# Kernel tuning notes

Hardware: AMD Instinct MI355X
Metric: run time of the kernel (lower is better)

The kernel has to match this reference:

```python
import jax, jax.numpy as jnp
import numpy as np

I = 256  # input size
H = 256  # hidden size
B = 128
S = 1024
EPS = 1e-5


def setup_inputs() -> dict:
    key = jax.random.key(0)
    ks = jax.random.split(key, 8)
    bound = 1.0 / np.sqrt(H)
    x = jax.random.normal(ks[0], (B, S, I), dtype=jnp.float32)
    mask = jax.random.randint(ks[1], (B, S), 0, 2) == 1
    W_ih = jax.random.uniform(ks[2], (4 * H, I), jnp.float32, -bound, bound)
    W_hh = jax.random.uniform(ks[3], (4 * H, H), jnp.float32, -bound, bound)
    b_ih = jax.random.uniform(ks[4], (4 * H,), jnp.float32, -bound, bound)
    b_hh = jax.random.uniform(ks[5], (4 * H,), jnp.float32, -bound, bound)
    gamma = jnp.ones((H,), jnp.float32)
    beta = jnp.zeros((H,), jnp.float32)
    return {"x": x, "mask": mask, "W_ih": W_ih, "W_hh": W_hh,
            "b_ih": b_ih, "b_hh": b_hh, "gamma": gamma, "beta": beta}


def _layernorm(h, gamma, beta):
    mu = jnp.mean(h, axis=-1, keepdims=True)
    var = jnp.var(h, axis=-1, keepdims=True)
    return (h - mu) * jax.lax.rsqrt(var + EPS) * gamma + beta


def reference(x, mask, W_ih, W_hh, b_ih, b_hh, gamma, beta):
    b = x.shape[0]
    h0 = jnp.zeros((b, H), x.dtype)
    c0 = jnp.zeros((b, H), x.dtype)
    out0 = jnp.zeros((b, H), x.dtype)

    def step(carry, inp):
        h, c, out = carry
        x_t, m_t = inp  # (B,I), (B,)
        hn = _layernorm(h, gamma, beta)
        gates = x_t @ W_ih.T + b_ih + hn @ W_hh.T + b_hh  # (B,4H)
        i_g, f_g, g_g, o_g = jnp.split(gates, 4, axis=-1)
        c = jax.nn.sigmoid(f_g) * c + jax.nn.sigmoid(i_g) * jnp.tanh(g_g)
        h = jax.nn.sigmoid(o_g) * jnp.tanh(c)
        # output[~mask] = h[~mask]; where mask is True the old output is kept
        out = jnp.where(m_t[:, None], out, h)
        return (h, c, out), None

    xs = (jnp.swapaxes(x, 0, 1), jnp.swapaxes(mask, 0, 1))  # (S,B,I), (S,B)
    (h, c, out), _ = jax.lax.scan(step, (h0, c0, out0), xs)
    return out
```

## Files before the change

### kernel.cpp

```cpp
#include <hip/hip_runtime.h>
#include <hip/hip_bf16.h>
#include <stdint.h>


#define Bb 128
#define Ss 1024
#define Ii 256
#define Hh 256
#define G4v 1024
#define EPSF 1e-5f

typedef __bf16 bf16;
typedef _Float16 f16;
typedef __attribute__((ext_vector_type(8))) __bf16 bf16x8;
typedef __attribute__((ext_vector_type(4))) __bf16 bf16x4;
typedef __attribute__((ext_vector_type(8))) _Float16 f16x8;
typedef __attribute__((ext_vector_type(4))) _Float16 f16x4;
typedef __attribute__((ext_vector_type(4))) float f32x4;
typedef unsigned int u32;
typedef unsigned long long u64;

static __device__ __forceinline__ f32x4 mfma16b(bf16x8 a, bf16x8 b, f32x4 c) {
  return __builtin_amdgcn_mfma_f32_16x16x32_bf16(a, b, c, 0, 0, 0);
}
static __device__ __forceinline__ f32x4 mfma16h(f16x8 a, f16x8 b, f32x4 c) {
  return __builtin_amdgcn_mfma_f32_16x16x32_f16(a, b, c, 0, 0, 0);
}
static __device__ __forceinline__ float sigm(float x) { return 1.0f / (1.0f + __expf(-x)); }
static __device__ __forceinline__ float tanhf_(float x) {
  float e = __expf(-2.0f * fabsf(x));
  float t = (1.0f - e) / (1.0f + e);
  return x < 0.0f ? -t : t;
}
static __device__ __forceinline__ unsigned short ush(f16 h) {
  return __builtin_bit_cast(unsigned short, h);
}
static __device__ __forceinline__ f16 hus(unsigned short u) {
  return __builtin_bit_cast(f16, u);
}

__global__ void k_conv_wih(const float* __restrict__ W, bf16* __restrict__ hi,
                           bf16* __restrict__ lo) {
  int i = (blockIdx.x * 256 + threadIdx.x) * 4;
  f32x4 v = *(const f32x4*)(W + i);
  bf16x4 h_, l_;
#pragma unroll
  for (int j = 0; j < 4; ++j) {
    bf16 hh = (bf16)v[j];
    h_[j] = hh;
    l_[j] = (bf16)(v[j] - (float)hh);
  }
  *(bf16x4*)(hi + i) = h_;
  *(bf16x4*)(lo + i) = l_;
}

__global__ void k_prep_whh(const float* __restrict__ W, const float* __restrict__ gamma,
                           f16* __restrict__ Wf) {
  int tid = blockIdx.x * 256 + threadIdx.x;
  int lane = tid & 63;
  int fk = tid >> 6;
  int ntg = fk >> 3, kt = fk & 7;
  int g = ntg * 16 + (lane & 15);
  int k = kt * 32 + ((lane >> 4) << 3);
  f16x8 r;
#pragma unroll
  for (int j = 0; j < 8; ++j) r[j] = (f16)(W[g * Hh + k + j] * gamma[k + j]);
  *(f16x8*)(Wf + (size_t)tid * 8) = r;
}

__global__ void k_prep_rd(const float* __restrict__ W, const float* __restrict__ gamma,
                          const float* __restrict__ beta, const float* __restrict__ bih,
                          const float* __restrict__ bhh, float* __restrict__ RD) {
  int g = blockIdx.x * 256 + threadIdx.x;
  float r = 0.f, d = 0.f;
  for (int k = 0; k < Hh; ++k) {
    float w = W[g * Hh + k];
    r += w * gamma[k];
    d += w * beta[k];
  }
  RD[2 * g] = r;
  RD[2 * g + 1] = d + bih[g] + bhh[g];
}

__global__ __launch_bounds__(256, 2) void k_gemm(const float* __restrict__ x,
                                                 const bf16* __restrict__ Whi,
                                                 const bf16* __restrict__ Wlo,
                                                 float* __restrict__ xw,
                                                 int t0, int Tc, int ntb) {
  __shared__ bf16 Bs[2][128 * 128];
  int bid = blockIdx.x;
  int b = bid & 127;
  int r2 = bid >> 7;
  int tb = r2 % ntb;
  int gt = r2 / ntb;
  int g0 = gt * 128;
  int tid = threadIdx.x, w = tid >> 6, lane = tid & 63;
  int li = lane & 15, lg = lane >> 4;
  char* BsB = (char*)Bs;
  int tbase = tb * 128 + 32 * w;
  f32x4 acc[2][8];
#pragma unroll
  for (int mt = 0; mt < 2; ++mt)
#pragma unroll
    for (int nt = 0; nt < 8; ++nt) acc[mt][nt] = (f32x4){0.f, 0.f, 0.f, 0.f};

  for (int kp = 0; kp < 2; ++kp) {
#pragma unroll
    for (int it = 0; it < 8; ++it) {
      int p = it * 4096 + tid * 16;
      int row = p >> 8, colb = p & 255;
      size_t goff = (size_t)(g0 + row) * 512 + kp * 256 + colb;
      int dst = row * 256 + (colb ^ ((row & 7) << 4));
      *(bf16x8*)(BsB + dst) = *(const bf16x8*)((const char*)Whi + goff);
      *(bf16x8*)(BsB + 32768 + dst) = *(const bf16x8*)((const char*)Wlo + goff);
    }
    __syncthreads();
#pragma unroll
    for (int kt = 0; kt < 4; ++kt) {
      int kl = kt * 32 + lg * 8;
      int kgl = kp * 128 + kl;
      bf16x8 ah[2], al[2];
#pragma unroll
      for (int mt = 0; mt < 2; ++mt) {
        int t = t0 + tbase + 16 * mt + li;
        const float* xp = x + ((size_t)b * Ss + t) * Ii + kgl;
        f32x4 f0 = *(const f32x4*)xp;
        f32x4 f1 = *(const f32x4*)(xp + 4);
        bf16x8 hv, lv;
#pragma unroll
        for (int j = 0; j < 4; ++j) {
          bf16 h0 = (bf16)f0[j];
          hv[j] = h0;
          lv[j] = (bf16)(f0[j] - (float)h0);
          bf16 h1 = (bf16)f1[j];
          hv[4 + j] = h1;
          lv[4 + j] = (bf16)(f1[j] - (float)h1);
        }
        ah[mt] = hv;
        al[mt] = lv;
      }
#pragma unroll
      for (int nt = 0; nt < 8; ++nt) {
        int grow = nt * 16 + li;
        int off = grow * 256 + ((kl * 2) ^ ((grow & 7) << 4));
        bf16x8 bh = *(const bf16x8*)(BsB + off);
        bf16x8 bl = *(const bf16x8*)(BsB + 32768 + off);
#pragma unroll
        for (int mt = 0; mt < 2; ++mt) {
          acc[mt][nt] = mfma16b(ah[mt], bh, acc[mt][nt]);
          acc[mt][nt] = mfma16b(ah[mt], bl, acc[mt][nt]);
          acc[mt][nt] = mfma16b(al[mt], bh, acc[mt][nt]);
        }
      }
    }
    __syncthreads();
  }
#pragma unroll
  for (int mt = 0; mt < 2; ++mt)
#pragma unroll
    for (int nt = 0; nt < 8; ++nt)
#pragma unroll
      for (int r = 0; r < 4; ++r) {
        int tl = tbase + 16 * mt + lg * 4 + r;
        int g = g0 + nt * 16 + li;
        xw[((size_t)b * Tc + tl) * G4v + g] = acc[mt][nt][r];
      }
}

__global__ __launch_bounds__(256, 1) void k_recur(
    const f16* __restrict__ Wf, const float* __restrict__ xw,
    const int* __restrict__ mask, const float* __restrict__ RD,
    float* __restrict__ st_h, float* __restrict__ st_c, float* __restrict__ st_o,
    u64* pub, float* __restrict__ out, int t0, int Tc, int first, int last) {
  __shared__ f16 hb[2][16 * 256];
  __shared__ float murs[2][16][2];
  __shared__ float2 spw[4][16];
  __shared__ float spart[16][16][2];
  int bid = blockIdx.x;
  int grp = bid & 7, q = bid >> 3;
  int tid = threadIdx.x, w = tid >> 6, lane = tid & 63;
  int li = lane & 15, lg = lane >> 4;
  int b0 = grp * 16;
  int jloc = (q * 4 + w) * 16 + li;
  char* hbB = (char*)hb;

  f16x8 wp[4][8];
#pragma unroll
  for (int c = 0; c < 4; ++c)
#pragma unroll
    for (int kt = 0; kt < 8; ++kt) {
      int ntg = c * 16 + q * 4 + w;
      wp[c][kt] = *(const f16x8*)(Wf + ((size_t)(ntg * 8 + kt) * 64 + lane) * 8);
      asm volatile("" : "+a"(wp[c][kt]));
    }
  float Rr[4], Dd[4];
#pragma unroll
  for (int c = 0; c < 4; ++c) {
    int g = c * 256 + jloc;
    Rr[c] = RD[2 * g];
    Dd[c] = RD[2 * g + 1];
  }

  float cst[4], ost[4];
  if (first) {
#pragma unroll
    for (int i = 0; i < 16; ++i) {
      hb[0][tid * 16 + i] = (f16)0.0f;
      hb[1][tid * 16 + i] = (f16)0.0f;
    }
#pragma unroll
    for (int r = 0; r < 4; ++r) { cst[r] = 0.f; ost[r] = 0.f; }
    if (tid < 16) { murs[0][tid][0] = 0.f; murs[0][tid][1] = rsqrtf(EPSF); }
  } else {
    int row = tid >> 4, cs = tid & 15, jseg = cs * 16;
    float s = 0.f, ss = 0.f;
#pragma unroll
    for (int i = 0; i < 16; ++i) {
      float v = st_h[(size_t)(b0 + row) * Hh + jseg + i];
      s += v;
      ss += v * v;
      f16 hh = (f16)v;
      int boff = row * 512 + (((jseg + i) * 2) ^ ((row & 7) << 4));
      *(f16*)(hbB + boff) = hh;
      *(f16*)(hbB + 8192 + boff) = (f16)(v - (float)hh);
    }
    spart[row][cs][0] = s;
    spart[row][cs][1] = ss;
#pragma unroll
    for (int r = 0; r < 4; ++r) {
      int m = lg * 4 + r;
      cst[r] = st_c[(size_t)(b0 + m) * Hh + jloc];
      ost[r] = st_o[(size_t)(b0 + m) * Hh + jloc];
    }
    __syncthreads();
    if (tid < 16) {
      float s2 = 0.f, ss2 = 0.f;
#pragma unroll
      for (int i = 0; i < 16; ++i) { s2 += spart[tid][i][0]; ss2 += spart[tid][i][1]; }
      float mu = s2 * (1.f / 256.f);
      float var = ss2 * (1.f / 256.f) - mu * mu;
      float rs = rsqrtf(var + EPSF);
      murs[0][tid][0] = mu * rs;
      murs[0][tid][1] = rs;
    }
  }
  __syncthreads();

  float xwv[4][4];
  int mk[4];
#pragma unroll
  for (int c = 0; c < 4; ++c)
#pragma unroll
    for (int r = 0; r < 4; ++r)
      xwv[c][r] = xw[((size_t)(b0 + lg * 4 + r) * Tc + 0) * G4v + c * 256 + jloc];
#pragma unroll
  for (int r = 0; r < 4; ++r) mk[r] = mask[(size_t)(b0 + lg * 4 + r) * Ss + t0];

  int grow = tid >> 4, gcg = tid & 15;

  for (int tl = 0; tl < Tc; ++tl) {
    int tg = t0 + tl;
    int slot = (tg + 1) & 1;
    u32 want = (u32)(tg + 1);

    f32x4 a0[4], a1[4];
#pragma unroll
    for (int c = 0; c < 4; ++c) {
      a0[c] = (f32x4){0.f, 0.f, 0.f, 0.f};
      a1[c] = (f32x4){0.f, 0.f, 0.f, 0.f};
    }
#pragma unroll
    for (int kt = 0; kt < 8; ++kt) {
      int aoff = li * 512 + (((kt * 32 + lg * 8) * 2) ^ ((li & 7) << 4));
      f16x8 ah = *(const f16x8*)(hbB + aoff);
      f16x8 al = *(const f16x8*)(hbB + 8192 + aoff);
#pragma unroll
      for (int c = 0; c < 4; ++c) {
        a0[c] = mfma16h(ah, wp[c][kt], a0[c]);
        a1[c] = mfma16h(al, wp[c][kt], a1[c]);
      }
    }
    float mrs[4], rsv[4];
#pragma unroll
    for (int r = 0; r < 4; ++r) {
      int m = lg * 4 + r;
      mrs[r] = murs[tl & 1][m][0];
      rsv[r] = murs[tl & 1][m][1];
    }
    __syncthreads();

    float hnew[4];
#pragma unroll
    for (int r = 0; r < 4; ++r) {
      float i_ = (a0[0][r] + a1[0][r]) * rsv[r] - mrs[r] * Rr[0] + Dd[0] + xwv[0][r];
      float f_ = (a0[1][r] + a1[1][r]) * rsv[r] - mrs[r] * Rr[1] + Dd[1] + xwv[1][r];
      float g_ = (a0[2][r] + a1[2][r]) * rsv[r] - mrs[r] * Rr[2] + Dd[2] + xwv[2][r];
      float o_ = (a0[3][r] + a1[3][r]) * rsv[r] - mrs[r] * Rr[3] + Dd[3] + xwv[3][r];
      float cn = sigm(f_) * cst[r] + sigm(i_) * tanhf_(g_);
      float hn = sigm(o_) * tanhf_(cn);
      cst[r] = cn;
      ost[r] = mk[r] ? ost[r] : hn;
      hnew[r] = hn;
    }
    u64* ph = pub + (size_t)(slot * 32 + bid) * 1024;
#pragma unroll
    for (int r = 0; r < 4; ++r) {
      int m = lg * 4 + r;
      float hn = hnew[r];
      f16 hh = (f16)hn;
      f16 hl = (f16)(hn - (float)hh);
      int boff = m * 512 + ((jloc * 2) ^ ((m & 7) << 4));
      *(f16*)(hbB + boff) = hh;
      *(f16*)(hbB + 8192 + boff) = hl;
      u64 pv = ((u64)want << 32) | ((u32)ush(hh) << 16) | (u32)ush(hl);
      __hip_atomic_store(&ph[m * 64 + (w * 16 + li)], pv, __ATOMIC_RELAXED,
                         __HIP_MEMORY_SCOPE_AGENT);
    }

    u64 gv[3][4];
    const u64* srcs[3];
#pragma unroll
    for (int pi = 0; pi < 3; ++pi) {
      int qq = (q + 1 + pi) & 3;
      int pbid = qq * 8 + grp;
      srcs[pi] = pub + (size_t)(slot * 32 + pbid) * 1024 + grow * 64 + gcg * 4;
#pragma unroll
      for (int e = 0; e < 4; ++e)
        gv[pi][e] = __hip_atomic_load(&srcs[pi][e], __ATOMIC_RELAXED,
                                      __HIP_MEMORY_SCOPE_AGENT);
    }

    {
      float sr[4], qr[4];
#pragma unroll
      for (int r = 0; r < 4; ++r) { sr[r] = hnew[r]; qr[r] = hnew[r] * hnew[r]; }
#pragma unroll
      for (int msk = 1; msk < 16; msk <<= 1)
#pragma unroll
        for (int r = 0; r < 4; ++r) {
          sr[r] += __shfl_xor(sr[r], msk);
          qr[r] += __shfl_xor(qr[r], msk);
        }
      if (li == 0)
#pragma unroll
        for (int r = 0; r < 4; ++r) spw[w][lg * 4 + r] = make_float2(sr[r], qr[r]);
    }
    if (tl == Tc - 1) {
#pragma unroll
      for (int r = 0; r < 4; ++r) {
        int m = lg * 4 + r;
        st_h[(size_t)(b0 + m) * Hh + jloc] = hnew[r];
        st_c[(size_t)(b0 + m) * Hh + jloc] = cst[r];
        st_o[(size_t)(b0 + m) * Hh + jloc] = ost[r];
      }
      if (last) {
#pragma unroll
        for (int r = 0; r < 4; ++r) out[(size_t)(b0 + lg * 4 + r) * Hh + jloc] = ost[r];
      }
    }
    {
      int tln = (tl + 1 < Tc) ? tl + 1 : Tc - 1;
#pragma unroll
      for (int c = 0; c < 4; ++c)
#pragma unroll
        for (int r = 0; r < 4; ++r)
          xwv[c][r] = xw[((size_t)(b0 + lg * 4 + r) * Tc + tln) * G4v + c * 256 + jloc];
#pragma unroll
      for (int r = 0; r < 4; ++r) mk[r] = mask[(size_t)(b0 + lg * 4 + r) * Ss + t0 + tln];
    }

    {
      u32 bad = 0;
#pragma unroll
      for (int pi = 0; pi < 3; ++pi)
#pragma unroll
        for (int e = 0; e < 4; ++e) bad |= (u32)(gv[pi][e] >> 32) ^ want;
      int cnt = 0;
      while (bad) {
#pragma unroll
        for (int pi = 0; pi < 3; ++pi)
#pragma unroll
          for (int e = 0; e < 4; ++e)
            gv[pi][e] = __hip_atomic_load(&srcs[pi][e], __ATOMIC_RELAXED,
                                          __HIP_MEMORY_SCOPE_AGENT);
        bad = 0;
#pragma unroll
        for (int pi = 0; pi < 3; ++pi)
#pragma unroll
          for (int e = 0; e < 4; ++e) bad |= (u32)(gv[pi][e] >> 32) ^ want;
        if (++cnt > (1 << 20)) break;
      }
    }
    float su = 0.f, qu = 0.f;
#pragma unroll
    for (int pi = 0; pi < 3; ++pi) {
      int qq = (q + 1 + pi) & 3;
      int j0 = qq * 64 + gcg * 4;
      int boff = grow * 512 + ((j0 * 2) ^ ((grow & 7) << 4));
      f16x4 h4, l4;
#pragma unroll
      for (int e = 0; e < 4; ++e) {
        u32 d = (u32)gv[pi][e];
        f16 hh = hus((unsigned short)(d >> 16));
        f16 hl = hus((unsigned short)(d & 0xffffu));
        h4[e] = hh;
        l4[e] = hl;
        float f = (float)hh + (float)hl;
        su += f;
        qu += f * f;
      }
      *(f16x4*)(hbB + boff) = h4;
      *(f16x4*)(hbB + 8192 + boff) = l4;
    }
#pragma unroll
    for (int msk = 1; msk < 16; msk <<= 1) {
      su += __shfl_xor(su, msk);
      qu += __shfl_xor(qu, msk);
    }
    __syncthreads();
    if (li == 0) {
      float s = su + spw[0][grow].x + spw[1][grow].x + spw[2][grow].x + spw[3][grow].x;
      float ss2 = qu + spw[0][grow].y + spw[1][grow].y + spw[2][grow].y + spw[3][grow].y;
      float mu = s * (1.f / 256.f);
      float var = ss2 * (1.f / 256.f) - mu * mu;
      float rs = rsqrtf(var + EPSF);
      murs[(tl + 1) & 1][grow][0] = mu * rs;
      murs[(tl + 1) & 1][grow][1] = rs;
    }
  }
}

extern "C" void kernel_launch(void* const* d_in, const int* in_sizes, int n_in,
                              void* d_out, int out_size, void* d_ws, size_t ws_size,
                              hipStream_t stream) {
  (void)in_sizes; (void)n_in; (void)out_size;
  const float* x = (const float*)d_in[0];
  const int* mask = (const int*)d_in[1];
  const float* Wih = (const float*)d_in[2];
  const float* Whh = (const float*)d_in[3];
  const float* bih = (const float*)d_in[4];
  const float* bhh = (const float*)d_in[5];
  const float* gamma = (const float*)d_in[6];
  const float* beta = (const float*)d_in[7];
  float* outp = (float*)d_out;
  char* ws = (char*)d_ws;

  const size_t extra = 3 * (512u << 10) + (8u << 10) + 3 * (128u << 10) +
                       (512u << 10) + (64u << 10);
  int Tc = 128;
  if (ws_size >= (size_t)1024 * 524288 + extra) Tc = 1024;
  else if (ws_size >= (size_t)512 * 524288 + extra) Tc = 512;
  else if (ws_size >= (size_t)256 * 524288 + extra) Tc = 256;

  size_t o = 0;
  auto take = [&](size_t bytes) { size_t r = o; o += (bytes + 255) & ~(size_t)255; return r; };
  size_t xw_off = take((size_t)Bb * Tc * G4v * 4);
  size_t wihh_off = take(512u << 10);
  size_t wihl_off = take(512u << 10);
  size_t whh_off = take(512u << 10);
  size_t rd_off = take(8u << 10);
  size_t sth_off = take(128u << 10);
  size_t stc_off = take(128u << 10);
  size_t sto_off = take(128u << 10);
  size_t pub_off = take(512u << 10);

  bf16* wihh = (bf16*)(ws + wihh_off);
  bf16* wihl = (bf16*)(ws + wihl_off);
  f16* whhf = (f16*)(ws + whh_off);
  float* rd = (float*)(ws + rd_off);
  float* xwp = (float*)(ws + xw_off);
  float* sth = (float*)(ws + sth_off);
  float* stc = (float*)(ws + stc_off);
  float* sto = (float*)(ws + sto_off);
  u64* pubh = (u64*)(ws + pub_off);

  hipMemsetAsync(pubh, 0, 512u << 10, stream);
  k_conv_wih<<<dim3(256), dim3(256), 0, stream>>>(Wih, wihh, wihl);
  k_prep_whh<<<dim3(128), dim3(256), 0, stream>>>(Whh, gamma, whhf);
  k_prep_rd<<<dim3(4), dim3(256), 0, stream>>>(Whh, gamma, beta, bih, bhh, rd);

  int nchunk = Ss / Tc;
  int ntb = Tc / 128;
  for (int ci = 0; ci < nchunk; ++ci) {
    int t0 = ci * Tc;
    k_gemm<<<dim3(8 * ntb * 128), dim3(256), 0, stream>>>(x, wihh, wihl, xwp, t0, Tc, ntb);
    k_recur<<<dim3(32), dim3(256), 0, stream>>>(whhf, xwp, mask, rd, sth, stc, sto,
                                                pubh, outp, t0, Tc,
                                                ci == 0 ? 1 : 0, ci == nchunk - 1 ? 1 : 0);
  }
}
```

Baseline: 4.757 ms.

## Interleave two batch groups per recurrent block to overlap exchange with compute

The recurrent kernel now runs 16 blocks instead of 32, and each block handles two 16-row batch groups (A and B) with the same register-resident W_hh fragments. Inside each timestep the block computes and publishes group A, then runs group B's MFMAs and gate math while A's cross-block hidden-state exchange is still in flight. It then waits for and ingests A's and B's peer data one after the other. The aim is to hide inter-block spin-wait and publish latency behind useful work, at the cost of twice the per-block serial compute, more registers, and extra barriers per step.

```diff
diff --git a/kernel.cpp b/kernel.cpp
--- a/kernel.cpp
+++ b/kernel.cpp
@@ -172,17 +172,19 @@
     const int* __restrict__ mask, const float* __restrict__ RD,
     float* __restrict__ st_h, float* __restrict__ st_c, float* __restrict__ st_o,
     u64* pub, float* __restrict__ out, int t0, int Tc, int first, int last) {
-  __shared__ f16 hb[2][16 * 256];
-  __shared__ float murs[2][16][2];
-  __shared__ float2 spw[4][16];
+  __shared__ f16 hbA[2][16 * 256];
+  __shared__ f16 hbB[2][16 * 256];
+  __shared__ float mursA[16][2], mursB[16][2];
+  __shared__ float2 spwA[4][16], spwB[4][16];
   __shared__ float spart[16][16][2];
   int bid = blockIdx.x;
-  int grp = bid & 7, q = bid >> 3;
+  int gp = bid & 3, q = bid >> 2;
   int tid = threadIdx.x, w = tid >> 6, lane = tid & 63;
   int li = lane & 15, lg = lane >> 4;
-  int b0 = grp * 16;
+  int b0A = gp * 16, b0B = (gp + 4) * 16;
   int jloc = (q * 4 + w) * 16 + li;
-  char* hbB = (char*)hb;
+  char* hbAB = (char*)hbA;
+  char* hbBB = (char*)hbB;
 
   f16x8 wp[4][8];
 #pragma unroll
@@ -201,60 +203,103 @@
     Dd[c] = RD[2 * g + 1];
   }
 
-  float cst[4], ost[4];
+  float cstA[4], ostA[4], cstB[4], ostB[4];
   if (first) {
 #pragma unroll
     for (int i = 0; i < 16; ++i) {
-      hb[0][tid * 16 + i] = (f16)0.0f;
-      hb[1][tid * 16 + i] = (f16)0.0f;
-    }
-#pragma unroll
-    for (int r = 0; r < 4; ++r) { cst[r] = 0.f; ost[r] = 0.f; }
-    if (tid < 16) { murs[0][tid][0] = 0.f; murs[0][tid][1] = rsqrtf(EPSF); }
+      hbA[0][tid * 16 + i] = (f16)0.0f;
+      hbA[1][tid * 16 + i] = (f16)0.0f;
+      hbB[0][tid * 16 + i] = (f16)0.0f;
+      hbB[1][tid * 16 + i] = (f16)0.0f;
+    }
+#pragma unroll
+    for (int r = 0; r < 4; ++r) { cstA[r] = 0.f; ostA[r] = 0.f; cstB[r] = 0.f; ostB[r] = 0.f; }
+    if (tid < 16) {
+      mursA[tid][0] = 0.f; mursA[tid][1] = rsqrtf(EPSF);
+      mursB[tid][0] = 0.f; mursB[tid][1] = rsqrtf(EPSF);
+    }
   } else {
     int row = tid >> 4, cs = tid & 15, jseg = cs * 16;
-    float s = 0.f, ss = 0.f;
-#pragma unroll
-    for (int i = 0; i < 16; ++i) {
-      float v = st_h[(size_t)(b0 + row) * Hh + jseg + i];
-      s += v;
-      ss += v * v;
-      f16 hh = (f16)v;
-      int boff = row * 512 + (((jseg + i) * 2) ^ ((row & 7) << 4));
-      *(f16*)(hbB + boff) = hh;
-      *(f16*)(hbB + 8192 + boff) = (f16)(v - (float)hh);
-    }
-    spart[row][cs][0] = s;
-    spart[row][cs][1] = ss;
+    {
+      float s = 0.f, ss = 0.f;
+#pragma unroll
+      for (int i = 0; i < 16; ++i) {
+        float v = st_h[(size_t)(b0A + row) * Hh + jseg + i];
+        s += v; ss += v * v;
+        f16 hh = (f16)v;
+        int boff = row * 512 + (((jseg + i) * 2) ^ ((row & 7) << 4));
+        *(f16*)(hbAB + boff) = hh;
+        *(f16*)(hbAB + 8192 + boff) = (f16)(v - (float)hh);
+      }
+      spart[row][cs][0] = s;
+      spart[row][cs][1] = ss;
+#pragma unroll
+      for (int r = 0; r < 4; ++r) {
+        int m = lg * 4 + r;
+        cstA[r] = st_c[(size_t)(b0A + m) * Hh + jloc];
+        ostA[r] = st_o[(size_t)(b0A + m) * Hh + jloc];
+      }
+      __syncthreads();
+      if (tid < 16) {
+        float s2 = 0.f, ss2 = 0.f;
+#pragma unroll
+        for (int i = 0; i < 16; ++i) { s2 += spart[tid][i][0]; ss2 += spart[tid][i][1]; }
+        float mu = s2 * (1.f / 256.f);
+        float var = ss2 * (1.f / 256.f) - mu * mu;
+        float rs = rsqrtf(var + EPSF);
+        mursA[tid][0] = mu * rs;
+        mursA[tid][1] = rs;
+      }
+      __syncthreads();
+    }
+    {
+      float s = 0.f, ss = 0.f;
+#pragma unroll
+      for (int i = 0; i < 16; ++i) {
+        float v = st_h[(size_t)(b0B + row) * Hh + jseg + i];
+        s += v; ss += v * v;
+        f16 hh = (f16)v;
+        int boff = row * 512 + (((jseg + i) * 2) ^ ((row & 7) << 4));
+        *(f16*)(hbBB + boff) = hh;
+        *(f16*)(hbBB + 8192 + boff) = (f16)(v - (float)hh);
+      }
+      spart[row][cs][0] = s;
+      spart[row][cs][1] = ss;
+#pragma unroll
+      for (int r = 0; r < 4; ++r) {
+        int m = lg * 4 + r;
+        cstB[r] = st_c[(size_t)(b0B + m) * Hh + jloc];
+        ostB[r] = st_o[(size_t)(b0B + m) * Hh + jloc];
+      }
+      __syncthreads();
+      if (tid < 16) {
+        float s2 = 0.f, ss2 = 0.f;
+#pragma unroll
+        for (int i = 0; i < 16; ++i) { s2 += spart[tid][i][0]; ss2 += spart[tid][i][1]; }
+        float mu = s2 * (1.f / 256.f);
+        float var = ss2 * (1.f / 256.f) - mu * mu;
+        float rs = rsqrtf(var + EPSF);
+        mursB[tid][0] = mu * rs;
+        mursB[tid][1] = rs;
+      }
+    }
+  }
+  __syncthreads();
+
+  float xwvA[4][4], xwvB[4][4];
+  int mkA[4], mkB[4];
+#pragma unroll
+  for (int c = 0; c < 4; ++c)
 #pragma unroll
     for (int r = 0; r < 4; ++r) {
-      int m = lg * 4 + r;
-      cst[r] = st_c[(size_t)(b0 + m) * Hh + jloc];
-      ost[r] = st_o[(size_t)(b0 + m) * Hh + jloc];
-    }
-    __syncthreads();
-    if (tid < 16) {
-      float s2 = 0.f, ss2 = 0.f;
-#pragma unroll
-      for (int i = 0; i < 16; ++i) { s2 += spart[tid][i][0]; ss2 += spart[tid][i][1]; }
-      float mu = s2 * (1.f / 256.f);
-      float var = ss2 * (1.f / 256.f) - mu * mu;
-      float rs = rsqrtf(var + EPSF);
-      murs[0][tid][0] = mu * rs;
-      murs[0][tid][1] = rs;
-    }
-  }
-  __syncthreads();
-
-  float xwv[4][4];
-  int mk[4];
-#pragma unroll
-  for (int c = 0; c < 4; ++c)
-#pragma unroll
-    for (int r = 0; r < 4; ++r)
-      xwv[c][r] = xw[((size_t)(b0 + lg * 4 + r) * Tc + 0) * G4v + c * 256 + jloc];
-#pragma unroll
-  for (int r = 0; r < 4; ++r) mk[r] = mask[(size_t)(b0 + lg * 4 + r) * Ss + t0];
+      xwvA[c][r] = xw[((size_t)(b0A + lg * 4 + r) * Tc + 0) * G4v + c * 256 + jloc];
+      xwvB[c][r] = xw[((size_t)(b0B + lg * 4 + r) * Tc + 0) * G4v + c * 256 + jloc];
+    }
+#pragma unroll
+  for (int r = 0; r < 4; ++r) {
+    mkA[r] = mask[(size_t)(b0A + lg * 4 + r) * Ss + t0];
+    mkB[r] = mask[(size_t)(b0B + lg * 4 + r) * Ss + t0];
+  }
 
   int grow = tid >> 4, gcg = tid & 15;
 
@@ -272,68 +317,50 @@
 #pragma unroll
     for (int kt = 0; kt < 8; ++kt) {
       int aoff = li * 512 + (((kt * 32 + lg * 8) * 2) ^ ((li & 7) << 4));
-      f16x8 ah = *(const f16x8*)(hbB + aoff);
-      f16x8 al = *(const f16x8*)(hbB + 8192 + aoff);
+      f16x8 ah = *(const f16x8*)(hbAB + aoff);
+      f16x8 al = *(const f16x8*)(hbAB + 8192 + aoff);
 #pragma unroll
       for (int c = 0; c < 4; ++c) {
         a0[c] = mfma16h(ah, wp[c][kt], a0[c]);
         a1[c] = mfma16h(al, wp[c][kt], a1[c]);
       }
     }
-    float mrs[4], rsv[4];
+    float mrsA[4], rsvA[4];
 #pragma unroll
     for (int r = 0; r < 4; ++r) {
       int m = lg * 4 + r;
-      mrs[r] = murs[tl & 1][m][0];
-      rsv[r] = murs[tl & 1][m][1];
+      mrsA[r] = mursA[m][0];
+      rsvA[r] = mursA[m][1];
     }
     __syncthreads();
 
-    float hnew[4];
-#pragma unroll
-    for (int r = 0; r < 4; ++r) {
-      float i_ = (a0[0][r] + a1[0][r]) * rsv[r] - mrs[r] * Rr[0] + Dd[0] + xwv[0][r];
-      float f_ = (a0[1][r] + a1[1][r]) * rsv[r] - mrs[r] * Rr[1] + Dd[1] + xwv[1][r];
-      float g_ = (a0[2][r] + a1[2][r]) * rsv[r] - mrs[r] * Rr[2] + Dd[2] + xwv[2][r];
-      float o_ = (a0[3][r] + a1[3][r]) * rsv[r] - mrs[r] * Rr[3] + Dd[3] + xwv[3][r];
-      float cn = sigm(f_) * cst[r] + sigm(i_) * tanhf_(g_);
-      float hn = sigm(o_) * tanhf_(cn);
-      cst[r] = cn;
-      ost[r] = mk[r] ? ost[r] : hn;
-      hnew[r] = hn;
-    }
-    u64* ph = pub + (size_t)(slot * 32 + bid) * 1024;
-#pragma unroll
-    for (int r = 0; r < 4; ++r) {
-      int m = lg * 4 + r;
-      float hn = hnew[r];
-      f16 hh = (f16)hn;
-      f16 hl = (f16)(hn - (float)hh);
-      int boff = m * 512 + ((jloc * 2) ^ ((m & 7) << 4));
-      *(f16*)(hbB + boff) = hh;
-      *(f16*)(hbB + 8192 + boff) = hl;
-      u64 pv = ((u64)want << 32) | ((u32)ush(hh) << 16) | (u32)ush(hl);
-      __hip_atomic_store(&ph[m * 64 + (w * 16 + li)], pv, __ATOMIC_RELAXED,
-                         __HIP_MEMORY_SCOPE_AGENT);
-    }
-
-    u64 gv[3][4];
-    const u64* srcs[3];
-#pragma unroll
-    for (int pi = 0; pi < 3; ++pi) {
-      int qq = (q + 1 + pi) & 3;
-      int pbid = qq * 8 + grp;
-      srcs[pi] = pub + (size_t)(slot * 32 + pbid) * 1024 + grow * 64 + gcg * 4;
-#pragma unroll
-      for (int e = 0; e < 4; ++e)
-        gv[pi][e] = __hip_atomic_load(&srcs[pi][e], __ATOMIC_RELAXED,
-                                      __HIP_MEMORY_SCOPE_AGENT);
-    }
-
+    float hnA[4];
     {
+      u64* ph = pub + (size_t)(slot * 32 + bid) * 1024;
+#pragma unroll
+      for (int r = 0; r < 4; ++r) {
+        float i_ = (a0[0][r] + a1[0][r]) * rsvA[r] - mrsA[r] * Rr[0] + Dd[0] + xwvA[0][r];
+        float f_ = (a0[1][r] + a1[1][r]) * rsvA[r] - mrsA[r] * Rr[1] + Dd[1] + xwvA[1][r];
+        float g_ = (a0[2][r] + a1[2][r]) * rsvA[r] - mrsA[r] * Rr[2] + Dd[2] + xwvA[2][r];
+        float o_ = (a0[3][r] + a1[3][r]) * rsvA[r] - mrsA[r] * Rr[3] + Dd[3] + xwvA[3][r];
+        float cn = sigm(f_) * cstA[r] + sigm(i_) * tanhf_(g_);
+        float hn = sigm(o_) * tanhf_(cn);
+        cstA[r] = cn;
+        ostA[r] = mkA[r] ? ostA[r] : hn;
+        hnA[r] = hn;
+        f16 hh = (f16)hn;
+        f16 hl = (f16)(hn - (float)hh);
+        int m = lg * 4 + r;
+        int boff = m * 512 + ((jloc * 2) ^ ((m & 7) << 4));
+        *(f16*)(hbAB + boff) = hh;
+        *(f16*)(hbAB + 8192 + boff) = hl;
+        u64 pv = ((u64)want << 32) | ((u32)ush(hh) << 16) | (u32)ush(hl);
+        __hip_atomic_store(&ph[m * 64 + (w * 16 + li)], pv, __ATOMIC_RELAXED,
+                           __HIP_MEMORY_SCOPE_AGENT);
+      }
       float sr[4], qr[4];
 #pragma unroll
-      for (int r = 0; r < 4; ++r) { sr[r] = hnew[r]; qr[r] = hnew[r] * hnew[r]; }
+      for (int r = 0; r < 4; ++r) { sr[r] = hnA[r]; qr[r] = hnA[r] * hnA[r]; }
 #pragma unroll
       for (int msk = 1; msk < 16; msk <<= 1)
 #pragma unroll
@@ -343,55 +370,149 @@
         }
       if (li == 0)
 #pragma unroll
-        for (int r = 0; r < 4; ++r) spw[w][lg * 4 + r] = make_float2(sr[r], qr[r]);
-    }
+        for (int r = 0; r < 4; ++r) spwA[w][lg * 4 + r] = make_float2(sr[r], qr[r]);
+    }
+
+    f32x4 c0[4], c1[4];
+#pragma unroll
+    for (int c = 0; c < 4; ++c) {
+      c0[c] = (f32x4){0.f, 0.f, 0.f, 0.f};
+      c1[c] = (f32x4){0.f, 0.f, 0.f, 0.f};
+    }
+#pragma unroll
+    for (int kt = 0; kt < 8; ++kt) {
+      int aoff = li * 512 + (((kt * 32 + lg * 8) * 2) ^ ((li & 7) << 4));
+      f16x8 ah = *(const f16x8*)(hbBB + aoff);
+      f16x8 al = *(const f16x8*)(hbBB + 8192 + aoff);
+#pragma unroll
+      for (int c = 0; c < 4; ++c) {
+        c0[c] = mfma16h(ah, wp[c][kt], c0[c]);
+        c1[c] = mfma16h(al, wp[c][kt], c1[c]);
+      }
+    }
+    float mrsB[4], rsvB[4];
+#pragma unroll
+    for (int r = 0; r < 4; ++r) {
+      int m = lg * 4 + r;
+      mrsB[r] = mursB[m][0];
+      rsvB[r] = mursB[m][1];
+    }
+    __syncthreads();
+
+    float hnB[4];
+    {
+      u64* ph = pub + (size_t)(slot * 32 + 16 + bid) * 1024;
+#pragma unroll
+      for (int r = 0; r < 4; ++r) {
+        float i_ = (c0[0][r] + c1[0][r]) * rsvB[r] - mrsB[r] * Rr[0] + Dd[0] + xwvB[0][r];
+        float f_ = (c0[1][r] + c1[1][r]) * rsvB[r] - mrsB[r] * Rr[1] + Dd[1] + xwvB[1][r];
+        float g_ = (c0[2][r] + c1[2][r]) * rsvB[r] - mrsB[r] * Rr[2] + Dd[2] + xwvB[2][r];
+        float o_ = (c0[3][r] + c1[3][r]) * rsvB[r] - mrsB[r] * Rr[3] + Dd[3] + xwvB[3][r];
+        float cn = sigm(f_) * cstB[r] + sigm(i_) * tanhf_(g_);
+        float hn = sigm(o_) * tanhf_(cn);
+        cstB[r] = cn;
+        ostB[r] = mkB[r] ? ostB[r] : hn;
+        hnB[r] = hn;
+        f16 hh = (f16)hn;
+        f16 hl = (f16)(hn - (float)hh);
+        int m = lg * 4 + r;
+        int boff = m * 512 + ((jloc * 2) ^ ((m & 7) << 4));
+        *(f16*)(hbBB + boff) = hh;
+        *(f16*)(hbBB + 8192 + boff) = hl;
+        u64 pv = ((u64)want << 32) | ((u32)ush(hh) << 16) | (u32)ush(hl);
+        __hip_atomic_store(&ph[m * 64 + (w * 16 + li)], pv, __ATOMIC_RELAXED,
+                           __HIP_MEMORY_SCOPE_AGENT);
+      }
+      float sr[4], qr[4];
+#pragma unroll
+      for (int r = 0; r < 4; ++r) { sr[r] = hnB[r]; qr[r] = hnB[r] * hnB[r]; }
+#pragma unroll
+      for (int msk = 1; msk < 16; msk <<= 1)
+#pragma unroll
+        for (int r = 0; r < 4; ++r) {
+          sr[r] += __shfl_xor(sr[r], msk);
+          qr[r] += __shfl_xor(qr[r], msk);
+        }
+      if (li == 0)
+#pragma unroll
+        for (int r = 0; r < 4; ++r) spwB[w][lg * 4 + r] = make_float2(sr[r], qr[r]);
+    }
+
     if (tl == Tc - 1) {
 #pragma unroll
       for (int r = 0; r < 4; ++r) {
         int m = lg * 4 + r;
-        st_h[(size_t)(b0 + m) * Hh + jloc] = hnew[r];
-        st_c[(size_t)(b0 + m) * Hh + jloc] = cst[r];
-        st_o[(size_t)(b0 + m) * Hh + jloc] = ost[r];
+        st_h[(size_t)(b0A + m) * Hh + jloc] = hnA[r];
+        st_c[(size_t)(b0A + m) * Hh + jloc] = cstA[r];
+        st_o[(size_t)(b0A + m) * Hh + jloc] = ostA[r];
+        st_h[(size_t)(b0B + m) * Hh + jloc] = hnB[r];
+        st_c[(size_t)(b0B + m) * Hh + jloc] = cstB[r];
+        st_o[(size_t)(b0B + m) * Hh + jloc] = ostB[r];
       }
       if (last) {
 #pragma unroll
-        for (int r = 0; r < 4; ++r) out[(size_t)(b0 + lg * 4 + r) * Hh + jloc] = ost[r];
-      }
+        for (int r = 0; r < 4; ++r) {
+          out[(size_t)(b0A + lg * 4 + r) * Hh + jloc] = ostA[r];
+          out[(size_t)(b0B + lg * 4 + r) * Hh + jloc] = ostB[r];
+        }
+      }
+    }
+
+    u64 gvA[3][4], gvB[3][4];
+    const u64* srcsA[3];
+    const u64* srcsB[3];
+#pragma unroll
+    for (int pi = 0; pi < 3; ++pi) {
+      int qq = (q + 1 + pi) & 3;
+      int pbid = qq * 4 + gp;
+      srcsA[pi] = pub + (size_t)(slot * 32 + pbid) * 1024 + grow * 64 + gcg * 4;
+      srcsB[pi] = pub + (size_t)(slot * 32 + 16 + pbid) * 1024 + grow * 64 + gcg * 4;
     }
     {
       int tln = (tl + 1 < Tc) ? tl + 1 : Tc - 1;
 #pragma unroll
       for (int c = 0; c < 4; ++c)
 #pragma unroll
-        for (int r = 0; r < 4; ++r)
-          xwv[c][r] = xw[((size_t)(b0 + lg * 4 + r) * Tc + tln) * G4v + c * 256 + jloc];
-#pragma unroll
-      for (int r = 0; r < 4; ++r) mk[r] = mask[(size_t)(b0 + lg * 4 + r) * Ss + t0 + tln];
-    }
+        for (int r = 0; r < 4; ++r) {
+          xwvA[c][r] = xw[((size_t)(b0A + lg * 4 + r) * Tc + tln) * G4v + c * 256 + jloc];
+          xwvB[c][r] = xw[((size_t)(b0B + lg * 4 + r) * Tc + tln) * G4v + c * 256 + jloc];
+        }
+#pragma unroll
+      for (int r = 0; r < 4; ++r) {
+        mkA[r] = mask[(size_t)(b0A + lg * 4 + r) * Ss + t0 + tln];
+        mkB[r] = mask[(size_t)(b0B + lg * 4 + r) * Ss + t0 + tln];
+      }
+    }
+#pragma unroll
+    for (int pi = 0; pi < 3; ++pi)
+#pragma unroll
+      for (int e = 0; e < 4; ++e)
+        gvA[pi][e] = __hip_atomic_load(&srcsA[pi][e], __ATOMIC_RELAXED,
+                                       __HIP_MEMORY_SCOPE_AGENT);
 
     {
       u32 bad = 0;
 #pragma unroll
       for (int pi = 0; pi < 3; ++pi)
 #pragma unroll
-        for (int e = 0; e < 4; ++e) bad |= (u32)(gv[pi][e] >> 32) ^ want;
+        for (int e = 0; e < 4; ++e) bad |= (u32)(gvA[pi][e] >> 32) ^ want;
       int cnt = 0;
       while (bad) {
 #pragma unroll
         for (int pi = 0; pi < 3; ++pi)
 #pragma unroll
           for (int e = 0; e < 4; ++e)
-            gv[pi][e] = __hip_atomic_load(&srcs[pi][e], __ATOMIC_RELAXED,
-                                          __HIP_MEMORY_SCOPE_AGENT);
+            gvA[pi][e] = __hip_atomic_load(&srcsA[pi][e], __ATOMIC_RELAXED,
+                                           __HIP_MEMORY_SCOPE_AGENT);
         bad = 0;
 #pragma unroll
         for (int pi = 0; pi < 3; ++pi)
 #pragma unroll
-          for (int e = 0; e < 4; ++e) bad |= (u32)(gv[pi][e] >> 32) ^ want;
+          for (int e = 0; e < 4; ++e) bad |= (u32)(gvA[pi][e] >> 32) ^ want;
         if (++cnt > (1 << 20)) break;
       }
     }
-    float su = 0.f, qu = 0.f;
+    float suA = 0.f, quA = 0.f;
 #pragma unroll
     for (int pi = 0; pi < 3; ++pi) {
       int qq = (q + 1 + pi) & 3;
@@ -400,32 +521,97 @@
       f16x4 h4, l4;
 #pragma unroll
       for (int e = 0; e < 4; ++e) {
-        u32 d = (u32)gv[pi][e];
+        u32 d = (u32)gvA[pi][e];
         f16 hh = hus((unsigned short)(d >> 16));
         f16 hl = hus((unsigned short)(d & 0xffffu));
         h4[e] = hh;
         l4[e] = hl;
         float f = (float)hh + (float)hl;
-        su += f;
-        qu += f * f;
-      }
-      *(f16x4*)(hbB + boff) = h4;
-      *(f16x4*)(hbB + 8192 + boff) = l4;
+        suA += f;
+        quA += f * f;
+      }
+      *(f16x4*)(hbAB + boff) = h4;
+      *(f16x4*)(hbAB + 8192 + boff) = l4;
     }
 #pragma unroll
     for (int msk = 1; msk < 16; msk <<= 1) {
-      su += __shfl_xor(su, msk);
-      qu += __shfl_xor(qu, msk);
-    }
+      suA += __shfl_xor(suA, msk);
+      quA += __shfl_xor(quA, msk);
+    }
+#pragma unroll
+    for (int pi = 0; pi < 3; ++pi)
+#pragma unroll
+      for (int e = 0; e < 4; ++e)
+        gvB[pi][e] = __hip_atomic_load(&srcsB[pi][e], __ATOMIC_RELAXED,
+                                       __HIP_MEMORY_SCOPE_AGENT);
     __syncthreads();
     if (li == 0) {
-      float s = su + spw[0][grow].x + spw[1][grow].x + spw[2][grow].x + spw[3][grow].x;
-      float ss2 = qu + spw[0][grow].y + spw[1][grow].y + spw[2][grow].y + spw[3][grow].y;
+      float s = suA + spwA[0][grow].x + spwA[1][grow].x + spwA[2][grow].x + spwA[3][grow].x;
+      float ss2 = quA + spwA[0][grow].y + spwA[1][grow].y + spwA[2][grow].y + spwA[3][grow].y;
       float mu = s * (1.f / 256.f);
       float var = ss2 * (1.f / 256.f) - mu * mu;
       float rs = rsqrtf(var + EPSF);
-      murs[(tl + 1) & 1][grow][0] = mu * rs;
-      murs[(tl + 1) & 1][grow][1] = rs;
+      mursA[grow][0] = mu * rs;
+      mursA[grow][1] = rs;
+    }
+
+    {
+      u32 bad = 0;
+#pragma unroll
+      for (int pi = 0; pi < 3; ++pi)
+#pragma unroll
+        for (int e = 0; e < 4; ++e) bad |= (u32)(gvB[pi][e] >> 32) ^ want;
+      int cnt = 0;
+      while (bad) {
+#pragma unroll
+        for (int pi = 0; pi < 3; ++pi)
+#pragma unroll
+          for (int e = 0; e < 4; ++e)
+            gvB[pi][e] = __hip_atomic_load(&srcsB[pi][e], __ATOMIC_RELAXED,
+                                           __HIP_MEMORY_SCOPE_AGENT);
+        bad = 0;
+#pragma unroll
+        for (int pi = 0; pi < 3; ++pi)
+#pragma unroll
+          for (int e = 0; e < 4; ++e) bad |= (u32)(gvB[pi][e] >> 32) ^ want;
+        if (++cnt > (1 << 20)) break;
+      }
+    }
+    float suB = 0.f, quB = 0.f;
+#pragma unroll
+    for (int pi = 0; pi < 3; ++pi) {
+      int qq = (q + 1 + pi) & 3;
+      int j0 = qq * 64 + gcg * 4;
+      int boff = grow * 512 + ((j0 * 2) ^ ((grow & 7) << 4));
+      f16x4 h4, l4;
+#pragma unroll
+      for (int e = 0; e < 4; ++e) {
+        u32 d = (u32)gvB[pi][e];
+        f16 hh = hus((unsigned short)(d >> 16));
+        f16 hl = hus((unsigned short)(d & 0xffffu));
+        h4[e] = hh;
+        l4[e] = hl;
+        float f = (float)hh + (float)hl;
+        suB += f;
+        quB += f * f;
+      }
+      *(f16x4*)(hbBB + boff) = h4;
+      *(f16x4*)(hbBB + 8192 + boff) = l4;
+    }
+#pragma unroll
+    for (int msk = 1; msk < 16; msk <<= 1) {
+      suB += __shfl_xor(suB, msk);
+      quB += __shfl_xor(quB, msk);
+    }
+    __syncthreads();
+    if (li == 0) {
+      float s = suB + spwB[0][grow].x + spwB[1][grow].x + spwB[2][grow].x + spwB[3][grow].x;
+      float ss2 = quB + spwB[0][grow].y + spwB[1][grow].y + spwB[2][grow].y + spwB[3][grow].y;
+      float mu = s * (1.f / 256.f);
+      float var = ss2 * (1.f / 256.f) - mu * mu;
+      float rs = rsqrtf(var + EPSF);
+      mursB[grow][0] = mu * rs;
+      mursB[grow][1] = rs;
     }
   }
 }
@@ -484,7 +670,7 @@
   for (int ci = 0; ci < nchunk; ++ci) {
     int t0 = ci * Tc;
     k_gemm<<<dim3(8 * ntb * 128), dim3(256), 0, stream>>>(x, wihh, wihl, xwp, t0, Tc, ntb);
-    k_recur<<<dim3(32), dim3(256), 0, stream>>>(whhf, xwp, mask, rd, sth, stc, sto,
+    k_recur<<<dim3(16), dim3(256), 0, stream>>>(whhf, xwp, mask, rd, sth, stc, sto,
                                                 pubh, outp, t0, Tc,
                                                 ci == 0 ? 1 : 0, ci == nchunk - 1 ? 1 : 0);
   }
```

Result: slower. 7.696 ms (+61.8%).
